# Performance work log

Hardware: AMD Instinct MI355X
Metric: run time of the kernel (lower is better)

The kernel has to match this reference:

```python
import jax, jax.numpy as jnp
import numpy as np

B, S, DK, DV = 32, 2048, 64, 64
TEMPERATURE = 8.0  # sqrt(d_k)
NEG_INF = -1e9


def setup_inputs() -> dict:
    key = jax.random.key(0)
    kq, kk, kv, km = jax.random.split(key, 4)
    q = jax.random.normal(kq, (B, S, DK), dtype=jnp.float32)
    k = jax.random.normal(kk, (B, S, DK), dtype=jnp.float32)
    v = jax.random.normal(kv, (B, S, DV), dtype=jnp.float32)
    mask = jax.random.randint(km, (B, S, S), 0, 2).astype(jnp.bool_)
    return {"q": q, "k": k, "v": v, "mask": mask}


def reference(q, k, v, mask):
    # attn scores: [B, Sq, Sk]
    attn = jnp.einsum('bqd,bkd->bqk', q, k) / TEMPERATURE
    attn = jnp.where(mask, NEG_INF, attn)
    attn = jax.nn.softmax(attn, axis=2)
    output = jnp.einsum('bqk,bkd->bqd', attn, v)  # [B, Sq, Dv]
    return (output, attn)
```

## Files before the change

kernel.cpp:

```cpp
#include <hip/hip_runtime.h>
#include <hip/hip_bf16.h>
#include <stdint.h>


#define B_ 32
#define S_ 2048
#define D_ 64

typedef float   f32x4  __attribute__((ext_vector_type(4)));
typedef __bf16  bf16x8 __attribute__((ext_vector_type(8)));
typedef unsigned short u16x4 __attribute__((ext_vector_type(4)));

__device__ __forceinline__ unsigned short f2bf(float f) {
  unsigned u = __float_as_uint(f);
  u = (u + 0x7FFFu + ((u >> 16) & 1u)) >> 16;
  return (unsigned short)u;
}

__device__ __forceinline__ unsigned pack2bf(float a, float b) {
  union { __bf16 h[2]; unsigned u; } r;
  r.h[0] = (__bf16)a; r.h[1] = (__bf16)b;
  return r.u;
}

__device__ __forceinline__ void load_lds16(const void* g, void* l) {
  __builtin_amdgcn_global_load_lds(
      (const __attribute__((address_space(1))) unsigned*)g,
      (__attribute__((address_space(3))) unsigned*)l, 16, 0, 0);
}

__global__ void detect_mask(const unsigned* __restrict__ m, int* __restrict__ flag) {
  if (threadIdx.x == 0 && blockIdx.x == 0) {
    int wide = 1;
    for (int i = 0; i < 64; ++i) {
      unsigned w = m[i];
      wide &= (w <= 1u || w == 0x3F800000u);
    }
    *flag = wide ? 1 : 0;
  }
}

__global__ void pack_mask(const void* __restrict__ M, const int* __restrict__ flag,
                          unsigned* __restrict__ Mp) {
  size_t t = (size_t)blockIdx.x * 256 + threadIdx.x;
  unsigned bits = 0;
  if (*flag == 0) {
    const uint4* p = (const uint4*)((const uint8_t*)M + t * 32);
    uint4 a = p[0], b = p[1];
    unsigned w[8] = {a.x, a.y, a.z, a.w, b.x, b.y, b.z, b.w};
#pragma unroll
    for (int i = 0; i < 8; ++i)
#pragma unroll
      for (int j = 0; j < 4; ++j)
        bits |= (unsigned)(((w[i] >> (8 * j)) & 0xFFu) != 0u) << (i * 4 + j);
  } else {
    const uint4* p = (const uint4*)((const unsigned*)M + t * 32);
#pragma unroll
    for (int i = 0; i < 8; ++i) {
      uint4 a = p[i];
      bits |= (unsigned)(a.x != 0u) << (i * 4 + 0);
      bits |= (unsigned)(a.y != 0u) << (i * 4 + 1);
      bits |= (unsigned)(a.z != 0u) << (i * 4 + 2);
      bits |= (unsigned)(a.w != 0u) << (i * 4 + 3);
    }
  }
  Mp[t] = bits;
}

__global__ void cast_k(const float* __restrict__ K, unsigned short* __restrict__ Kbf) {
  size_t i = ((size_t)blockIdx.x * 256 + threadIdx.x) * 4;
  f32x4 v = *reinterpret_cast<const f32x4*>(K + i);
  u16x4 o;
  o[0] = f2bf(v[0]); o[1] = f2bf(v[1]); o[2] = f2bf(v[2]); o[3] = f2bf(v[3]);
  *reinterpret_cast<u16x4*>(Kbf + i) = o;
}

__global__ void transpose_v(const float* __restrict__ V, unsigned short* __restrict__ Vt) {
  __shared__ float tile[32][33];
  int b = blockIdx.z, k0 = blockIdx.x * 32, d0 = blockIdx.y * 32;
  int tx = threadIdx.x, ty = threadIdx.y;
  const float* src = V + ((size_t)b * S_ + k0) * D_ + d0;
  for (int r = 0; r < 4; ++r) {
    int yy = ty + r * 8;
    tile[yy][tx] = src[(size_t)yy * D_ + tx];
  }
  __syncthreads();
  unsigned short* dst = Vt + ((size_t)b * D_ + d0) * S_ + k0;
  for (int r = 0; r < 4; ++r) {
    int yy = ty + r * 8;
    dst[(size_t)yy * S_ + tx] = f2bf(tile[tx][yy]);
  }
}

#define MFMA16(A, B, C) __builtin_amdgcn_mfma_f32_16x16x32_bf16(A, B, C, 0, 0, 0)

__global__ __launch_bounds__(256, 4) void attn_main5(
    const float* __restrict__ Q, const unsigned short* __restrict__ Kbf,
    const unsigned* __restrict__ Mp, const unsigned short* __restrict__ Vt,
    float* __restrict__ Out) {
  __shared__ __align__(16) unsigned short smem[16384];

  const int t = threadIdx.x;
  int wg = blockIdx.x;
  int vdx = (wg & 7) * 128 + (wg >> 3);
  int b = vdx >> 5, qt = vdx & 31;
  int wave = t >> 6, lane = t & 63;
  int q0 = qt * 64 + wave * 16;
  const int lo = lane & 15, hi = lane >> 4;
  const int s0 = lo + (((2 * hi) & 3) << 4);
  const int s1 = lo + (((2 * hi + 1) & 3) << 4);
  const bool hl = hi < 2;

  const unsigned short* Kb  = Kbf + (size_t)b * S_ * D_;
  const unsigned short* Vtb = Vt  + (size_t)b * D_ * S_;
  const unsigned* mptr = Mp + ((size_t)b * S_ + q0 + lo) * (S_ / 32);
  float* outO = Out + (size_t)b * S_ * D_;
  float* sp   = Out + (size_t)B_ * S_ * D_ + ((size_t)b * S_ + q0 + lo) * S_;

  bf16x8 bq0, bq1;
  {
    const float* qr = Q + ((size_t)b * S_ + q0 + lo) * D_ + hi * 8;
    f32x4 x0 = *reinterpret_cast<const f32x4*>(qr);
    f32x4 y0 = *reinterpret_cast<const f32x4*>(qr + 4);
    f32x4 x1 = *reinterpret_cast<const f32x4*>(qr + 32);
    f32x4 y1 = *reinterpret_cast<const f32x4*>(qr + 36);
#pragma unroll
    for (int j = 0; j < 4; ++j) {
      bq0[j] = (__bf16)(x0[j] * 0.125f); bq0[j + 4] = (__bf16)(y0[j] * 0.125f);
      bq1[j] = (__bf16)(x1[j] * 0.125f); bq1[j + 4] = (__bf16)(y1[j] * 0.125f);
    }
  }

  const int sr = t >> 3, sj = t & 7;
  const unsigned short* kg = Kb  + (size_t)sr * D_ + ((sj ^ (sr & 7)) << 3);
  const unsigned short* vg = Vtb + (size_t)sr * S_ + ((sj ^ (sr & 7)) << 3);

  const int sw = lo & 7;
  const int offA0 = lo * 64 + ((hi ^ sw) << 3);
  const int offA1 = lo * 64 + (((hi + 4) ^ sw) << 3);

  float lsum = 0.f;
#pragma unroll
  for (int c = 0; c < 4; ++c)
    load_lds16(kg + (size_t)c * 32 * D_, &smem[c * 2048 + t * 8]);
  __syncthreads();

  for (int kc = 0; kc < 16; ++kc) {
    const int cur = kc & 1;
    if (kc < 15) {
      const unsigned short* src = kg + (size_t)(kc + 1) * 128 * D_;
      unsigned short* dst = &smem[(cur ^ 1) * 8192 + t * 8];
#pragma unroll
      for (int c = 0; c < 4; ++c)
        load_lds16(src + (size_t)c * 32 * D_, dst + c * 2048);
    }
    unsigned mwz[4];
#pragma unroll
    for (int w = 0; w < 4; ++w) mwz[w] = mptr[4 * kc + w];
    const unsigned short* kl = &smem[cur * 8192];

    __builtin_amdgcn_s_setprio(1);
    f32x4 a[8];
#pragma unroll
    for (int g = 0; g < 8; ++g) {
      bf16x8 A0 = *reinterpret_cast<const bf16x8*>(kl + g * 1024 + offA0);
      bf16x8 A1 = *reinterpret_cast<const bf16x8*>(kl + g * 1024 + offA1);
      f32x4 acc = {0.f, 0.f, 0.f, 0.f};
      acc = MFMA16(A0, bq0, acc);
      a[g] = MFMA16(A1, bq1, acc);
    }
    __builtin_amdgcn_s_setprio(0);

#pragma unroll
    for (int g = 0; g < 8; ++g) {
      unsigned bits = mwz[g >> 1] >> ((g & 1) * 16);
#pragma unroll
      for (int i = 0; i < 4; ++i)
        lsum += ((bits >> (4 * hi + i)) & 1u) ? 0.f : __expf(a[g][i]);
    }
    __syncthreads();
  }

  lsum += __shfl_xor(lsum, 16, 64);
  lsum += __shfl_xor(lsum, 32, 64);
  const float rinv = 1.0f / lsum;

  f32x4 oacc[4];
#pragma unroll
  for (int db = 0; db < 4; ++db) {
    oacc[db][0] = 0.f; oacc[db][1] = 0.f; oacc[db][2] = 0.f; oacc[db][3] = 0.f;
  }

#pragma unroll
  for (int c = 0; c < 2; ++c) {
    load_lds16(kg + (size_t)c * 32 * D_, &smem[c * 2048 + t * 8]);
    load_lds16(vg + (size_t)c * 32 * S_, &smem[8192 + c * 2048 + t * 8]);
  }
  __syncthreads();

  for (int kc = 0; kc < 32; ++kc) {
    const int cur = kc & 1;
    if (kc < 31) {
      const unsigned short* ks = kg + (size_t)(kc + 1) * 64 * D_;
      const unsigned short* vs = vg + (kc + 1) * 64;
      unsigned short* kd = &smem[(cur ^ 1) * 4096 + t * 8];
      unsigned short* vd = &smem[8192 + (cur ^ 1) * 4096 + t * 8];
#pragma unroll
      for (int c = 0; c < 2; ++c) {
        load_lds16(ks + (size_t)c * 32 * D_, kd + c * 2048);
        load_lds16(vs + (size_t)c * 32 * S_, vd + c * 2048);
      }
    }
    unsigned mw0 = mptr[2 * kc], mw1 = mptr[2 * kc + 1];
    const unsigned short* kl = &smem[cur * 4096];
    const unsigned short* vl = &smem[8192 + cur * 4096];

    __builtin_amdgcn_s_setprio(1);
    f32x4 a[4];
#pragma unroll
    for (int g = 0; g < 4; ++g) {
      bf16x8 A0 = *reinterpret_cast<const bf16x8*>(kl + g * 1024 + offA0);
      bf16x8 A1 = *reinterpret_cast<const bf16x8*>(kl + g * 1024 + offA1);
      f32x4 acc = {0.f, 0.f, 0.f, 0.f};
      acc = MFMA16(A0, bq0, acc);
      a[g] = MFMA16(A1, bq1, acc);
    }
    __builtin_amdgcn_s_setprio(0);

#pragma unroll
    for (int H = 0; H < 2; ++H) {
      const unsigned bits = (H == 0) ? mw0 : mw1;
      f32x4 p0, p1;
#pragma unroll
      for (int i = 0; i < 4; ++i) {
        p0[i] = ((bits >> (4 * hi + i)) & 1u) ? 0.f
                : __expf(a[2 * H][i]) * rinv;
        p1[i] = ((bits >> (16 + 4 * hi + i)) & 1u) ? 0.f
                : __expf(a[2 * H + 1][i]) * rinv;
      }
      __builtin_nontemporal_store(p0,
          reinterpret_cast<f32x4*>(sp + kc * 64 + H * 32 + 4 * hi));
      __builtin_nontemporal_store(p1,
          reinterpret_cast<f32x4*>(sp + kc * 64 + H * 32 + 16 + 4 * hi));

      unsigned pk0 = pack2bf(p0[0], p0[1]), pk1 = pack2bf(p0[2], p0[3]);
      unsigned pk2 = pack2bf(p1[0], p1[1]), pk3 = pack2bf(p1[2], p1[3]);
      unsigned t00 = (unsigned)__shfl((int)pk0, s0, 64);
      unsigned t20 = (unsigned)__shfl((int)pk2, s0, 64);
      unsigned t10 = (unsigned)__shfl((int)pk1, s0, 64);
      unsigned t30 = (unsigned)__shfl((int)pk3, s0, 64);
      unsigned t01 = (unsigned)__shfl((int)pk0, s1, 64);
      unsigned t21 = (unsigned)__shfl((int)pk2, s1, 64);
      unsigned t11 = (unsigned)__shfl((int)pk1, s1, 64);
      unsigned t31 = (unsigned)__shfl((int)pk3, s1, 64);
      uint4 dw;
      dw.x = hl ? t00 : t20; dw.y = hl ? t10 : t30;
      dw.z = hl ? t01 : t21; dw.w = hl ? t11 : t31;
      bf16x8 pa = __builtin_bit_cast(bf16x8, dw);

      const int offV = (H == 0) ? offA0 : offA1;
      __builtin_amdgcn_s_setprio(1);
#pragma unroll
      for (int db = 0; db < 4; ++db) {
        bf16x8 bv = *reinterpret_cast<const bf16x8*>(vl + db * 1024 + offV);
        oacc[db] = MFMA16(pa, bv, oacc[db]);
      }
      __builtin_amdgcn_s_setprio(0);
    }
    __syncthreads();
  }

#pragma unroll
  for (int db = 0; db < 4; ++db)
#pragma unroll
    for (int i = 0; i < 4; ++i)
      __builtin_nontemporal_store(oacc[db][i],
          outO + (size_t)(q0 + hi * 4 + i) * D_ + db * 16 + lo);
}

extern "C" void kernel_launch(void* const* d_in, const int* in_sizes, int n_in,
                              void* d_out, int out_size, void* d_ws, size_t ws_size,
                              hipStream_t stream) {
  const float* q = (const float*)d_in[0];
  const float* k = (const float*)d_in[1];
  const float* v = (const float*)d_in[2];
  const void*  m = d_in[3];
  float* out = (float*)d_out;

  int* flag = (int*)d_ws;
  unsigned short* Vt  = (unsigned short*)((char*)d_ws + 256);
  unsigned short* Kbf = (unsigned short*)((char*)d_ws + 256 + (size_t)B_ * D_ * S_ * 2);
  unsigned*       Mp  = (unsigned*)((char*)d_ws + 256 + (size_t)B_ * D_ * S_ * 4);

  detect_mask<<<1, 64, 0, stream>>>((const unsigned*)m, flag);
  cast_k<<<(B_ * S_ * D_) / (256 * 4), 256, 0, stream>>>(k, Kbf);
  transpose_v<<<dim3(S_ / 32, D_ / 32, B_), dim3(32, 8), 0, stream>>>(v, Vt);
  pack_mask<<<(B_ * S_ * (S_ / 32)) / 256, 256, 0, stream>>>(m, flag, Mp);
  attn_main5<<<B_ * (S_ / 64), 256, 0, stream>>>(q, Kbf, Mp, Vt, out);
}
```

Before: 376.3 us.

## Fuse prep kernels and switch attention to single-wave workgroups with fine-grained pipelining

After: 446.4 us. 18.6% more time.

```diff
diff --git a/kernel.cpp b/kernel.cpp
--- a/kernel.cpp
+++ b/kernel.cpp
@@ -7,20 +7,20 @@
 #define S_ 2048
 #define D_ 64
 
-typedef float   f32x4  __attribute__((ext_vector_type(4)));
-typedef __bf16  bf16x8 __attribute__((ext_vector_type(8)));
+typedef float  f32x4  __attribute__((ext_vector_type(4)));
+typedef __bf16 bf16x8 __attribute__((ext_vector_type(8)));
+typedef __bf16 bf16x4 __attribute__((ext_vector_type(4)));
 typedef unsigned short u16x4 __attribute__((ext_vector_type(4)));
+
+#define WAITV(N) do { asm volatile("s_waitcnt vmcnt(" N ")" ::: "memory"); \
+                      __builtin_amdgcn_sched_barrier(0); } while (0)
+#define WAITL()  do { asm volatile("s_waitcnt lgkmcnt(0)" ::: "memory");   \
+                      __builtin_amdgcn_sched_barrier(0); } while (0)
 
 __device__ __forceinline__ unsigned short f2bf(float f) {
   unsigned u = __float_as_uint(f);
   u = (u + 0x7FFFu + ((u >> 16) & 1u)) >> 16;
   return (unsigned short)u;
-}
-
-__device__ __forceinline__ unsigned pack2bf(float a, float b) {
-  union { __bf16 h[2]; unsigned u; } r;
-  r.h[0] = (__bf16)a; r.h[1] = (__bf16)b;
-  return r.u;
 }
 
 __device__ __forceinline__ void load_lds16(const void* g, void* l) {
@@ -40,76 +40,77 @@
   }
 }
 
-__global__ void pack_mask(const void* __restrict__ M, const int* __restrict__ flag,
-                          unsigned* __restrict__ Mp) {
-  size_t t = (size_t)blockIdx.x * 256 + threadIdx.x;
-  unsigned bits = 0;
-  if (*flag == 0) {
-    const uint4* p = (const uint4*)((const uint8_t*)M + t * 32);
-    uint4 a = p[0], b = p[1];
-    unsigned w[8] = {a.x, a.y, a.z, a.w, b.x, b.y, b.z, b.w};
-#pragma unroll
-    for (int i = 0; i < 8; ++i)
-#pragma unroll
-      for (int j = 0; j < 4; ++j)
-        bits |= (unsigned)(((w[i] >> (8 * j)) & 0xFFu) != 0u) << (i * 4 + j);
+__global__ __launch_bounds__(256) void prep_fused(
+    const float* __restrict__ K, unsigned short* __restrict__ Kbf,
+    const float* __restrict__ V, unsigned short* __restrict__ Vt,
+    const void* __restrict__ M, const int* __restrict__ flag,
+    unsigned* __restrict__ Mp) {
+  __shared__ float tile[32][33];
+  const int bid = blockIdx.x, tid = threadIdx.x;
+
+  if (bid < 4096) {
+    size_t i = ((size_t)bid * 256 + tid) * 4;
+    f32x4 v = *reinterpret_cast<const f32x4*>(K + i);
+    u16x4 o;
+    o[0] = f2bf(v[0]); o[1] = f2bf(v[1]); o[2] = f2bf(v[2]); o[3] = f2bf(v[3]);
+    *reinterpret_cast<u16x4*>(Kbf + i) = o;
+  } else if (bid < 8192) {
+    int b2 = bid - 4096;
+    int k0 = (b2 & 63) * 32, d0 = ((b2 >> 6) & 1) * 32, b = b2 >> 7;
+    int tx = tid & 31, ty = tid >> 5;
+    const float* src = V + ((size_t)b * S_ + k0) * D_ + d0;
+    for (int r = 0; r < 4; ++r) {
+      int yy = ty + r * 8;
+      tile[yy][tx] = src[(size_t)yy * D_ + tx];
+    }
+    __syncthreads();
+    unsigned short* dst = Vt + ((size_t)b * D_ + d0) * S_ + k0;
+    for (int r = 0; r < 4; ++r) {
+      int yy = ty + r * 8;
+      dst[(size_t)yy * S_ + tx] = f2bf(tile[tx][yy]);
+    }
   } else {
-    const uint4* p = (const uint4*)((const unsigned*)M + t * 32);
-#pragma unroll
-    for (int i = 0; i < 8; ++i) {
-      uint4 a = p[i];
-      bits |= (unsigned)(a.x != 0u) << (i * 4 + 0);
-      bits |= (unsigned)(a.y != 0u) << (i * 4 + 1);
-      bits |= (unsigned)(a.z != 0u) << (i * 4 + 2);
-      bits |= (unsigned)(a.w != 0u) << (i * 4 + 3);
-    }
-  }
-  Mp[t] = bits;
-}
-
-__global__ void cast_k(const float* __restrict__ K, unsigned short* __restrict__ Kbf) {
-  size_t i = ((size_t)blockIdx.x * 256 + threadIdx.x) * 4;
-  f32x4 v = *reinterpret_cast<const f32x4*>(K + i);
-  u16x4 o;
-  o[0] = f2bf(v[0]); o[1] = f2bf(v[1]); o[2] = f2bf(v[2]); o[3] = f2bf(v[3]);
-  *reinterpret_cast<u16x4*>(Kbf + i) = o;
-}
-
-__global__ void transpose_v(const float* __restrict__ V, unsigned short* __restrict__ Vt) {
-  __shared__ float tile[32][33];
-  int b = blockIdx.z, k0 = blockIdx.x * 32, d0 = blockIdx.y * 32;
-  int tx = threadIdx.x, ty = threadIdx.y;
-  const float* src = V + ((size_t)b * S_ + k0) * D_ + d0;
-  for (int r = 0; r < 4; ++r) {
-    int yy = ty + r * 8;
-    tile[yy][tx] = src[(size_t)yy * D_ + tx];
-  }
-  __syncthreads();
-  unsigned short* dst = Vt + ((size_t)b * D_ + d0) * S_ + k0;
-  for (int r = 0; r < 4; ++r) {
-    int yy = ty + r * 8;
-    dst[(size_t)yy * S_ + tx] = f2bf(tile[tx][yy]);
+    size_t t = (size_t)(bid - 8192) * 256 + tid;
+    unsigned bits = 0;
+    if (*flag == 0) {
+      const uint4* p = (const uint4*)((const uint8_t*)M + t * 32);
+      uint4 a = p[0], b = p[1];
+      unsigned w[8] = {a.x, a.y, a.z, a.w, b.x, b.y, b.z, b.w};
+#pragma unroll
+      for (int i = 0; i < 8; ++i)
+#pragma unroll
+        for (int j = 0; j < 4; ++j)
+          bits |= (unsigned)(((w[i] >> (8 * j)) & 0xFFu) != 0u) << (i * 4 + j);
+    } else {
+      const uint4* p = (const uint4*)((const unsigned*)M + t * 32);
+#pragma unroll
+      for (int i = 0; i < 8; ++i) {
+        uint4 a = p[i];
+        bits |= (unsigned)(a.x != 0u) << (i * 4 + 0);
+        bits |= (unsigned)(a.y != 0u) << (i * 4 + 1);
+        bits |= (unsigned)(a.z != 0u) << (i * 4 + 2);
+        bits |= (unsigned)(a.w != 0u) << (i * 4 + 3);
+      }
+    }
+    Mp[t] = bits;
   }
 }
 
 #define MFMA16(A, B, C) __builtin_amdgcn_mfma_f32_16x16x32_bf16(A, B, C, 0, 0, 0)
 
-__global__ __launch_bounds__(256, 4) void attn_main5(
+__global__ __launch_bounds__(64) void attn_main7(
     const float* __restrict__ Q, const unsigned short* __restrict__ Kbf,
     const unsigned* __restrict__ Mp, const unsigned short* __restrict__ Vt,
     float* __restrict__ Out) {
-  __shared__ __align__(16) unsigned short smem[16384];
-
-  const int t = threadIdx.x;
-  int wg = blockIdx.x;
-  int vdx = (wg & 7) * 128 + (wg >> 3);
-  int b = vdx >> 5, qt = vdx & 31;
-  int wave = t >> 6, lane = t & 63;
-  int q0 = qt * 64 + wave * 16;
+  __shared__ __align__(16) unsigned short smem[4096];
+
+  const int wg = blockIdx.x;
+  const int vdx = (wg & 7) * 512 + (wg >> 3);
+  const int b = vdx >> 7, qt = vdx & 127;
+  const int q0 = qt * 16;
+  const int lane = threadIdx.x;
   const int lo = lane & 15, hi = lane >> 4;
-  const int s0 = lo + (((2 * hi) & 3) << 4);
-  const int s1 = lo + (((2 * hi + 1) & 3) << 4);
-  const bool hl = hi < 2;
+  const int sw = lo & 7;
 
   const unsigned short* Kb  = Kbf + (size_t)b * S_ * D_;
   const unsigned short* Vtb = Vt  + (size_t)b * D_ * S_;
@@ -131,55 +132,53 @@
     }
   }
 
-  const int sr = t >> 3, sj = t & 7;
-  const unsigned short* kg = Kb  + (size_t)sr * D_ + ((sj ^ (sr & 7)) << 3);
-  const unsigned short* vg = Vtb + (size_t)sr * S_ + ((sj ^ (sr & 7)) << 3);
-
-  const int sw = lo & 7;
-  const int offA0 = lo * 64 + ((hi ^ sw) << 3);
-  const int offA1 = lo * 64 + (((hi + 4) ^ sw) << 3);
+  const int krow = lane >> 3;
+  const int kcol = ((lane & 7) ^ krow) << 3;
+  const int vrow = lane >> 1;
+  const int vcol = (lane & 1) << 3;
+
+  const int offK0 = ((hi ^ sw) << 3);
+  const int offK1 = (((hi + 4) ^ sw) << 3);
 
   float lsum = 0.f;
-#pragma unroll
-  for (int c = 0; c < 4; ++c)
-    load_lds16(kg + (size_t)c * 32 * D_, &smem[c * 2048 + t * 8]);
-  __syncthreads();
-
-  for (int kc = 0; kc < 16; ++kc) {
-    const int cur = kc & 1;
-    if (kc < 15) {
-      const unsigned short* src = kg + (size_t)(kc + 1) * 128 * D_;
-      unsigned short* dst = &smem[(cur ^ 1) * 8192 + t * 8];
-#pragma unroll
-      for (int c = 0; c < 4; ++c)
-        load_lds16(src + (size_t)c * 32 * D_, dst + c * 2048);
-    }
-    unsigned mwz[4];
-#pragma unroll
-    for (int w = 0; w < 4; ++w) mwz[w] = mptr[4 * kc + w];
-    const unsigned short* kl = &smem[cur * 8192];
-
-    __builtin_amdgcn_s_setprio(1);
-    f32x4 a[8];
-#pragma unroll
-    for (int g = 0; g < 8; ++g) {
-      bf16x8 A0 = *reinterpret_cast<const bf16x8*>(kl + g * 1024 + offA0);
-      bf16x8 A1 = *reinterpret_cast<const bf16x8*>(kl + g * 1024 + offA1);
-      f32x4 acc = {0.f, 0.f, 0.f, 0.f};
-      acc = MFMA16(A0, bq0, acc);
-      a[g] = MFMA16(A1, bq1, acc);
-    }
-    __builtin_amdgcn_s_setprio(0);
-
-#pragma unroll
-    for (int g = 0; g < 8; ++g) {
-      unsigned bits = mwz[g >> 1] >> ((g & 1) * 16);
-#pragma unroll
-      for (int i = 0; i < 4; ++i)
-        lsum += ((bits >> (4 * hi + i)) & 1u) ? 0.f : __expf(a[g][i]);
-    }
-    __syncthreads();
-  }
+
+#define STAGE_K1(t_, buf_)                                                  \
+  {                                                                         \
+    const unsigned short* s_ = Kb + (size_t)((t_) * 32 + krow) * D_ + kcol; \
+    unsigned short* d_ = &smem[(buf_) * 2048];                              \
+    load_lds16(s_,                d_);                                      \
+    load_lds16(s_ +  8 * D_,      d_ +  512);                               \
+    load_lds16(s_ + 16 * D_,      d_ + 1024);                               \
+    load_lds16(s_ + 24 * D_,      d_ + 1536);                               \
+  }
+
+#define COMP32(t_, buf_)                                                    \
+  {                                                                         \
+    const unsigned short* kl = &smem[(buf_) * 2048];                        \
+    unsigned mw = mptr[(t_)];                                               \
+    _Pragma("unroll")                                                       \
+    for (int h = 0; h < 2; ++h) {                                           \
+      const unsigned short* kr = kl + (h * 16 + lo) * 64;                   \
+      bf16x8 A0 = *reinterpret_cast<const bf16x8*>(kr + offK0);             \
+      bf16x8 A1 = *reinterpret_cast<const bf16x8*>(kr + offK1);             \
+      f32x4 acc = {0.f, 0.f, 0.f, 0.f};                                     \
+      acc = MFMA16(A0, bq0, acc);                                           \
+      acc = MFMA16(A1, bq1, acc);                                           \
+      unsigned bits = mw >> (h * 16);                                       \
+      _Pragma("unroll")                                                     \
+      for (int i = 0; i < 4; ++i)                                           \
+        lsum += ((bits >> (4 * hi + i)) & 1u) ? 0.f : __expf(acc[i]);       \
+    }                                                                       \
+  }
+
+  STAGE_K1(0, 0);
+  for (int t = 0; t < 63; ++t) {
+    STAGE_K1(t + 1, (t + 1) & 1);
+    WAITV("4");
+    COMP32(t, t & 1);
+  }
+  WAITV("0");
+  COMP32(63, 1);
 
   lsum += __shfl_xor(lsum, 16, 64);
   lsum += __shfl_xor(lsum, 32, 64);
@@ -191,83 +190,71 @@
     oacc[db][0] = 0.f; oacc[db][1] = 0.f; oacc[db][2] = 0.f; oacc[db][3] = 0.f;
   }
 
-#pragma unroll
-  for (int c = 0; c < 2; ++c) {
-    load_lds16(kg + (size_t)c * 32 * D_, &smem[c * 2048 + t * 8]);
-    load_lds16(vg + (size_t)c * 32 * S_, &smem[8192 + c * 2048 + t * 8]);
-  }
-  __syncthreads();
-
-  for (int kc = 0; kc < 32; ++kc) {
-    const int cur = kc & 1;
-    if (kc < 31) {
-      const unsigned short* ks = kg + (size_t)(kc + 1) * 64 * D_;
-      const unsigned short* vs = vg + (kc + 1) * 64;
-      unsigned short* kd = &smem[(cur ^ 1) * 4096 + t * 8];
-      unsigned short* vd = &smem[8192 + (cur ^ 1) * 4096 + t * 8];
-#pragma unroll
-      for (int c = 0; c < 2; ++c) {
-        load_lds16(ks + (size_t)c * 32 * D_, kd + c * 2048);
-        load_lds16(vs + (size_t)c * 32 * S_, vd + c * 2048);
-      }
-    }
-    unsigned mw0 = mptr[2 * kc], mw1 = mptr[2 * kc + 1];
-    const unsigned short* kl = &smem[cur * 4096];
-    const unsigned short* vl = &smem[8192 + cur * 4096];
-
-    __builtin_amdgcn_s_setprio(1);
-    f32x4 a[4];
-#pragma unroll
-    for (int g = 0; g < 4; ++g) {
-      bf16x8 A0 = *reinterpret_cast<const bf16x8*>(kl + g * 1024 + offA0);
-      bf16x8 A1 = *reinterpret_cast<const bf16x8*>(kl + g * 1024 + offA1);
+#define STAGE_KV2(u_, buf_)                                                 \
+  {                                                                         \
+    const unsigned short* ks = Kb + (size_t)((u_) * 16 + krow) * D_ + kcol; \
+    unsigned short* kd = &smem[(buf_) * 1024];                              \
+    load_lds16(ks,           kd);                                           \
+    load_lds16(ks + 8 * D_,  kd + 512);                                     \
+    const unsigned short* vs = Vtb + (size_t)vrow * S_ + (u_) * 16 + vcol;  \
+    unsigned short* vd = &smem[2048 + (buf_) * 1024];                       \
+    load_lds16(vs,            vd);                                          \
+    load_lds16(vs + 32 * S_,  vd + 512);                                    \
+  }
+
+  const bf16x4 zed = {(__bf16)0.f, (__bf16)0.f, (__bf16)0.f, (__bf16)0.f};
+
+  WAITL();
+  STAGE_KV2(0, 0);
+
+  for (int g = 0; g < 32; ++g) {
+    f32x4 pb0, pb1, pb2, pb3;
+#pragma unroll
+    for (int j = 0; j < 4; ++j) {
+      const int u = g * 4 + j;
+      if (u < 127) STAGE_KV2(u + 1, (u + 1) & 1);
+      if (u == 127)      { WAITV("0"); }
+      else if (j != 0)   { WAITV("4"); }
+      else if (g == 0)   { WAITV("4"); }
+      else               { WAITV("8"); }
+
+      const unsigned short* kl = &smem[(u & 1) * 1024];
+      const unsigned short* vl = &smem[2048 + (u & 1) * 1024];
+
+      const unsigned short* kr = kl + lo * 64;
+      bf16x8 A0 = *reinterpret_cast<const bf16x8*>(kr + offK0);
+      bf16x8 A1 = *reinterpret_cast<const bf16x8*>(kr + offK1);
       f32x4 acc = {0.f, 0.f, 0.f, 0.f};
       acc = MFMA16(A0, bq0, acc);
-      a[g] = MFMA16(A1, bq1, acc);
-    }
-    __builtin_amdgcn_s_setprio(0);
-
-#pragma unroll
-    for (int H = 0; H < 2; ++H) {
-      const unsigned bits = (H == 0) ? mw0 : mw1;
-      f32x4 p0, p1;
-#pragma unroll
-      for (int i = 0; i < 4; ++i) {
-        p0[i] = ((bits >> (4 * hi + i)) & 1u) ? 0.f
-                : __expf(a[2 * H][i]) * rinv;
-        p1[i] = ((bits >> (16 + 4 * hi + i)) & 1u) ? 0.f
-                : __expf(a[2 * H + 1][i]) * rinv;
-      }
-      __builtin_nontemporal_store(p0,
-          reinterpret_cast<f32x4*>(sp + kc * 64 + H * 32 + 4 * hi));
-      __builtin_nontemporal_store(p1,
-          reinterpret_cast<f32x4*>(sp + kc * 64 + H * 32 + 16 + 4 * hi));
-
-      unsigned pk0 = pack2bf(p0[0], p0[1]), pk1 = pack2bf(p0[2], p0[3]);
-      unsigned pk2 = pack2bf(p1[0], p1[1]), pk3 = pack2bf(p1[2], p1[3]);
-      unsigned t00 = (unsigned)__shfl((int)pk0, s0, 64);
-      unsigned t20 = (unsigned)__shfl((int)pk2, s0, 64);
-      unsigned t10 = (unsigned)__shfl((int)pk1, s0, 64);
-      unsigned t30 = (unsigned)__shfl((int)pk3, s0, 64);
-      unsigned t01 = (unsigned)__shfl((int)pk0, s1, 64);
-      unsigned t21 = (unsigned)__shfl((int)pk2, s1, 64);
-      unsigned t11 = (unsigned)__shfl((int)pk1, s1, 64);
-      unsigned t31 = (unsigned)__shfl((int)pk3, s1, 64);
-      uint4 dw;
-      dw.x = hl ? t00 : t20; dw.y = hl ? t10 : t30;
-      dw.z = hl ? t01 : t21; dw.w = hl ? t11 : t31;
-      bf16x8 pa = __builtin_bit_cast(bf16x8, dw);
-
-      const int offV = (H == 0) ? offA0 : offA1;
-      __builtin_amdgcn_s_setprio(1);
+      acc = MFMA16(A1, bq1, acc);
+
+      unsigned mword = mptr[u >> 1];
+      unsigned bits = (u & 1) ? (mword >> 16) : (mword & 0xFFFFu);
+      f32x4 p;
+#pragma unroll
+      for (int i = 0; i < 4; ++i)
+        p[i] = ((bits >> (4 * hi + i)) & 1u) ? 0.f : __expf(acc[i]) * rinv;
+
+      if (j == 0) pb0 = p; else if (j == 1) pb1 = p;
+      else if (j == 2) pb2 = p; else pb3 = p;
+
+      bf16x4 pc;
+#pragma unroll
+      for (int i = 0; i < 4; ++i) pc[i] = (__bf16)p[i];
+      bf16x8 pa = __builtin_shufflevector(pc, zed, 0, 1, 2, 3, 4, 5, 6, 7);
 #pragma unroll
       for (int db = 0; db < 4; ++db) {
-        bf16x8 bv = *reinterpret_cast<const bf16x8*>(vl + db * 1024 + offV);
+        bf16x4 vv = *reinterpret_cast<const bf16x4*>(
+            vl + (db * 16 + lo) * 16 + hi * 4);
+        bf16x8 bv = __builtin_shufflevector(vv, zed, 0, 1, 2, 3, 4, 5, 6, 7);
         oacc[db] = MFMA16(pa, bv, oacc[db]);
       }
-      __builtin_amdgcn_s_setprio(0);
-    }
-    __syncthreads();
+    }
+    float* spg = sp + g * 64 + 4 * hi;
+    __builtin_nontemporal_store(pb0, reinterpret_cast<f32x4*>(spg));
+    __builtin_nontemporal_store(pb1, reinterpret_cast<f32x4*>(spg + 16));
+    __builtin_nontemporal_store(pb2, reinterpret_cast<f32x4*>(spg + 32));
+    __builtin_nontemporal_store(pb3, reinterpret_cast<f32x4*>(spg + 48));
   }
 
 #pragma unroll
@@ -275,7 +262,7 @@
 #pragma unroll
     for (int i = 0; i < 4; ++i)
       __builtin_nontemporal_store(oacc[db][i],
-          outO + (size_t)(q0 + hi * 4 + i) * D_ + db * 16 + lo);
+          outO + (size_t)(q0 + 4 * hi + i) * D_ + db * 16 + lo);
 }
 
 extern "C" void kernel_launch(void* const* d_in, const int* in_sizes, int n_in,
@@ -293,8 +280,6 @@
   unsigned*       Mp  = (unsigned*)((char*)d_ws + 256 + (size_t)B_ * D_ * S_ * 4);
 
   detect_mask<<<1, 64, 0, stream>>>((const unsigned*)m, flag);
-  cast_k<<<(B_ * S_ * D_) / (256 * 4), 256, 0, stream>>>(k, Kbf);
-  transpose_v<<<dim3(S_ / 32, D_ / 32, B_), dim3(32, 8), 0, stream>>>(v, Vt);
-  pack_mask<<<(B_ * S_ * (S_ / 32)) / 256, 256, 0, stream>>>(m, flag, Mp);
-  attn_main5<<<B_ * (S_ / 64), 256, 0, stream>>>(q, Kbf, Mp, Vt, out);
-}
+  prep_fused<<<24576, 256, 0, stream>>>(k, Kbf, v, Vt, m, flag, Mp);
+  attn_main7<<<B_ * (S_ / 16), 64, 0, stream>>>(q, Kbf, Mp, Vt, out);
+}
```
